# Optimization experiments

Hardware: AMD Instinct MI355X
Metric: run time of the kernel (lower is better)

## Reference

```python
import jax, jax.numpy as jnp
import numpy as np

B, L, D = 2, 2048, 1024
H = 16
DH = D // H  # 64


def rope_tables(seq_len, dim):
    # inv_freq: [dim/2]
    inv_freq = 1.0 / (10000.0 ** (jnp.arange(0, dim, 2, dtype=jnp.float32) / dim))
    t = jnp.arange(seq_len, dtype=jnp.float32)
    freqs = jnp.outer(t, inv_freq)            # [L, dim/2]
    emb = jnp.concatenate([freqs, freqs], -1)  # [L, dim]
    return jnp.cos(emb), jnp.sin(emb)


def rotate_half(x):
    x1, x2 = x[..., : x.shape[-1] // 2], x[..., x.shape[-1] // 2 :]
    return jnp.concatenate([-x2, x1], axis=-1)


def setup_inputs() -> dict:
    key = jax.random.key(0)
    k1, k2, k3 = jax.random.split(key, 3)
    x = jax.random.normal(k1, (B, L, D), dtype=jnp.float32)
    # nn.Linear weight init scale ~ 1/sqrt(fan_in)
    Wqkv = jax.random.normal(k2, (D, 3 * D), dtype=jnp.float32) / np.sqrt(D)
    Wo = jax.random.normal(k3, (D, D), dtype=jnp.float32) / np.sqrt(D)
    return {"x": x, "Wqkv": Wqkv, "Wo": Wo}


def reference(x, Wqkv, Wo):
    b, l, d = x.shape
    qkv = (x @ Wqkv).reshape(b, l, 3, H, DH)
    q, k, v = qkv[:, :, 0], qkv[:, :, 1], qkv[:, :, 2]  # [B, L, H, DH]

    cos, sin = rope_tables(l, DH)          # [L, DH]
    cos = cos[:, None, :]                   # [L, 1, DH] broadcast over heads
    sin = sin[:, None, :]
    q = q * cos + rotate_half(q) * sin
    k = k * cos + rotate_half(k) * sin

    scale = DH ** -0.5
    # full (non-causal) attention, faithful to the source
    scores = jnp.einsum("bqhd,bkhd->bhqk", q, k) * scale   # [B, H, L, L]
    attn = jax.nn.softmax(scores, axis=-1)
    out = jnp.einsum("bhqk,bkhd->bqhd", attn, v)            # [B, L, H, DH]
    out = out.reshape(b, l, d)
    return out @ Wo
```

## Files before the change

### kernel.cpp

```cpp
#include <hip/hip_runtime.h>
#include <hip/hip_bf16.h>

#define B_  2
#define L_  2048
#define D_  1024
#define H_  16
#define DH_ 64
#define M_  (B_*L_)
#define N1_ (3*D_)

#define QSCALE (0.125f * 1.44269504088896340736f)

typedef __bf16 bf16x8 __attribute__((ext_vector_type(8)));
typedef float  f32x4  __attribute__((ext_vector_type(4)));
typedef unsigned short ushort_t;
typedef unsigned short ushort8_t __attribute__((ext_vector_type(8)));
typedef unsigned int   uintx2    __attribute__((ext_vector_type(2)));

#define MFMA16(a,b,c) __builtin_amdgcn_mfma_f32_16x16x32_bf16((a),(b),(c),0,0,0)

__device__ __forceinline__ float4 ld4(const float* p) { return *(const float4*)p; }

__device__ __forceinline__ ushort_t f2bf(float f) {
    union { float f; unsigned int u; } v; v.f = f;
    unsigned int r = (v.u + 0x7FFFu + ((v.u >> 16) & 1u)) >> 16;
    return (ushort_t)r;
}
__device__ __forceinline__ float bf2f(ushort_t u) {
    union { unsigned int u; float f; } v; v.u = ((unsigned int)u) << 16;
    return v.f;
}
__device__ __forceinline__ float exp2_(float x) {
    float r; asm("v_exp_f32 %0, %1" : "=v"(r) : "v"(x)); return r;
}
__device__ __forceinline__ float fract_(float x) {
    float r; asm("v_fract_f32 %0, %1" : "=v"(r) : "v"(x)); return r;
}
__device__ __forceinline__ float sin_rev(float x) {
    float r; asm("v_sin_f32 %0, %1" : "=v"(r) : "v"(x)); return r;
}
__device__ __forceinline__ float cos_rev(float x) {
    float r; asm("v_cos_f32 %0, %1" : "=v"(r) : "v"(x)); return r;
}
__device__ __forceinline__ unsigned cvtpk(float a, float b) {
    unsigned r; asm("v_cvt_pk_bf16_f32 %0, %1, %2" : "=v"(r) : "v"(a), "v"(b)); return r;
}
__device__ __forceinline__ float bperm_f(int byte_addr, float v) {
    union { float f; int i; } u; u.f = v;
    u.i = __builtin_amdgcn_ds_bpermute(byte_addr, u.i);
    return u.f;
}
__device__ __forceinline__ void gload16(const ushort_t* g, ushort_t* l) {
    __builtin_amdgcn_global_load_lds(
        (const __attribute__((address_space(1))) unsigned int*)g,
        (__attribute__((address_space(3))) unsigned int*)l, 16, 0, 0);
}

__global__ __launch_bounds__(256)
void prep(const float* __restrict__ x, const float* __restrict__ Wqkv,
          const float* __restrict__ Wo,
          ushort_t* __restrict__ xb, ushort_t* __restrict__ wqt,
          ushort_t* __restrict__ wot)
{
    __shared__ float vs[64][65];
    const int bid = blockIdx.x, t = threadIdx.x;
    if (bid < 2048) {
        int i = (bid * 256 + t) * 8;
        float4 a = ld4(x + i), b = ld4(x + i + 4);
        ushort8_t o;
        o[0] = f2bf(a.x); o[1] = f2bf(a.y); o[2] = f2bf(a.z); o[3] = f2bf(a.w);
        o[4] = f2bf(b.x); o[5] = f2bf(b.y); o[6] = f2bf(b.z); o[7] = f2bf(b.w);
        *(ushort8_t*)(xb + i) = o;
        return;
    }
    const float* in; ushort_t* out; int nt, kt, N;
    if (bid < 2048 + 768) {
        in = Wqkv; out = wqt; N = N1_;
        nt = (bid - 2048) % 48; kt = (bid - 2048) / 48;
    } else {
        in = Wo; out = wot; N = D_;
        nt = (bid - 2816) % 16; kt = (bid - 2816) / 16;
    }
    #pragma unroll
    for (int i = 0; i < 4; ++i) {
        int idx = t + 256 * i;
        int row = idx >> 4, c4 = idx & 15;
        float4 x4 = ld4(in + (size_t)(kt * 64 + row) * N + nt * 64 + c4 * 4);
        vs[row][c4*4+0] = x4.x; vs[row][c4*4+1] = x4.y;
        vs[row][c4*4+2] = x4.z; vs[row][c4*4+3] = x4.w;
    }
    __syncthreads();
    #pragma unroll
    for (int i = 0; i < 16; ++i) {
        int idx = t + 256 * i;
        int nc = idx >> 6, kc = idx & 63;
        out[(size_t)(nt * 64 + nc) * 1024 + kt * 64 + kc] = f2bf(vs[kc][nc]);
    }
}

template<int EPI, int BM, int NXB, int NWG>
__global__ __launch_bounds__(256)
void bgemm(const ushort_t* __restrict__ A, const ushort_t* __restrict__ Bt,
           float* __restrict__ Cf,
           ushort_t* __restrict__ Qo, ushort_t* __restrict__ Ko, ushort_t* __restrict__ Vo)
{
    constexpr int K  = 1024;
    constexpr int MI = BM / 32;
    __shared__ ushort_t As[BM * 64];
    __shared__ ushort_t Bs[128 * 64];
    const int t  = threadIdx.x;
    const int l  = t & 63, w = t >> 6;
    const int g  = l >> 4, ln = l & 15;
    const int wr = w >> 1, wc = w & 1;
    const int bid = blockIdx.x;
    const int lid = (bid & 7) * (NWG / 8) + (bid >> 3);
    const int m0 = (lid / NXB) * BM, n0 = (lid % NXB) * 128;

    const int srow = w * 8 + (l >> 3);
    const int sch  = (l & 7) ^ (l >> 3);
    const ushort_t* Ag = A  + ((size_t)(m0 + srow)) * K + sch * 8;
    const ushort_t* Bg = Bt + ((size_t)(n0 + srow)) * K + sch * 8;

    f32x4 acc[MI][4];
    #pragma unroll
    for (int mi = 0; mi < MI; ++mi)
        #pragma unroll
        for (int nj = 0; nj < 4; ++nj) acc[mi][nj] = f32x4{0.f, 0.f, 0.f, 0.f};

    for (int kt = 0; kt < K / 64; ++kt) {
        #pragma unroll
        for (int i = 0; i < BM / 32; ++i)
            gload16(Ag + (size_t)i * 32 * K + kt * 64, &As[i * 2048 + w * 512]);
        #pragma unroll
        for (int i = 0; i < 4; ++i)
            gload16(Bg + (size_t)i * 32 * K + kt * 64, &Bs[i * 2048 + w * 512]);
        __syncthreads();

        #pragma unroll
        for (int kk = 0; kk < 2; ++kk) {
            bf16x8 af[MI], bfv[4];
            #pragma unroll
            for (int mi = 0; mi < MI; ++mi) {
                int row  = (BM / 2) * wr + 16 * mi + ln;
                int phys = (4 * kk + g) ^ (ln & 7);
                af[mi] = *(const bf16x8*)&As[row * 64 + phys * 8];
            }
            #pragma unroll
            for (int nj = 0; nj < 4; ++nj) {
                int row  = 64 * wc + 16 * nj + ln;
                int phys = (4 * kk + g) ^ (ln & 7);
                bfv[nj] = *(const bf16x8*)&Bs[row * 64 + phys * 8];
            }
            #pragma unroll
            for (int mi = 0; mi < MI; ++mi)
                #pragma unroll
                for (int nj = 0; nj < 4; ++nj)
                    acc[mi][nj] = MFMA16(af[mi], bfv[nj], acc[mi][nj]);
        }
        __syncthreads();
    }

    if (EPI == 0) {
        #pragma unroll
        for (int mi = 0; mi < MI; ++mi) {
            #pragma unroll
            for (int nj = 0; nj < 4; ++nj) {
                int n = n0 + 64 * wc + 16 * nj + ln;
                #pragma unroll
                for (int r = 0; r < 4; ++r) {
                    int m = m0 + (BM / 2) * wr + 16 * mi + 4 * g + r;
                    Cf[(size_t)m * D_ + n] = acc[mi][nj][r];
                }
            }
        }
    } else {
        const int nb    = n0 + 64 * wc;
        const int which = nb >> 10;
        const int h     = (nb >> 6) & (H_ - 1);
        if (which == 2) {
            #pragma unroll
            for (int mi = 0; mi < MI; ++mi)
                #pragma unroll
                for (int nj = 0; nj < 4; ++nj) {
                    int dh = 16 * nj + ln;
                    #pragma unroll
                    for (int r = 0; r < 4; ++r) {
                        int m = m0 + (BM / 2) * wr + 16 * mi + 4 * g + r;
                        int b = m >> 11, ll = m & (L_ - 1);
                        Vo[((size_t)(b * H_ + h) * DH_ + dh) * L_ + ll] = f2bf(acc[mi][nj][r]);
                    }
                }
        } else {
            ushort_t* base = (which == 0) ? Qo : Ko;
            const float scale = (which == 0) ? QSCALE : 1.0f;
            const float invr0 = exp2_(-(float)ln        * 0.41524101186f) * 0.15915494310f;
            const float invr1 = exp2_(-(float)(16 + ln) * 0.41524101186f) * 0.15915494310f;
            #pragma unroll
            for (int mi = 0; mi < MI; ++mi) {
                #pragma unroll
                for (int r = 0; r < 4; ++r) {
                    int m = m0 + (BM / 2) * wr + 16 * mi + 4 * g + r;
                    int b = m >> 11, ll = m & (L_ - 1);
                    float rv0 = fract_((float)ll * invr0);
                    float rv1 = fract_((float)ll * invr1);
                    float s0 = sin_rev(rv0), c0 = cos_rev(rv0);
                    float s1 = sin_rev(rv1), c1 = cos_rev(rv1);
                    size_t rb = ((size_t)(b * H_ + h) * L_ + ll) * DH_;
                    float a1 = acc[mi][0][r], a2 = acc[mi][2][r];
                    base[rb + ln]      = f2bf((a1 * c0 - a2 * s0) * scale);
                    base[rb + ln + 32] = f2bf((a2 * c0 + a1 * s0) * scale);
                    float b1 = acc[mi][1][r], b2 = acc[mi][3][r];
                    base[rb + 16 + ln]      = f2bf((b1 * c1 - b2 * s1) * scale);
                    base[rb + 16 + ln + 32] = f2bf((b2 * c1 + b1 * s1) * scale);
                }
            }
        }
    }
}

__global__ __launch_bounds__(256)
void attn_mfma(const ushort_t* __restrict__ qb, const ushort_t* __restrict__ kb,
               const ushort_t* __restrict__ vt, ushort_t* __restrict__ ao)
{
    __shared__ ushort_t Ks[128 * 64];
    __shared__ ushort_t Vs[64 * 128];
    __shared__ ushort_t Ps[4][32 * 64];

    const int t    = threadIdx.x;
    const int lane = t & 63, wv = t >> 6;
    const int g    = lane >> 4, ln = lane & 15;
    const int bid  = blockIdx.x;
    const int lid  = (bid & 7) * 64 + (bid >> 3);
    const int bh   = lid >> 4;
    const int q0   = (lid & 15) * 128 + wv * 32;

    const ushort_t* qpA = qb + ((size_t)bh * L_ + q0 + ln) * DH_;
    bf16x8 qf[2][2];
    qf[0][0] = *(const bf16x8*)(qpA + 8 * g);
    qf[0][1] = *(const bf16x8*)(qpA + 32 + 8 * g);
    qf[1][0] = *(const bf16x8*)(qpA + 16 * DH_ + 8 * g);
    qf[1][1] = *(const bf16x8*)(qpA + 16 * DH_ + 32 + 8 * g);

    const ushort_t* kp = kb + (size_t)bh * L_ * DH_;
    const ushort_t* vp = vt + (size_t)bh * DH_ * L_;

    union { ushort8_t u; bf16x8 v; } onesu;
    #pragma unroll
    for (int j = 0; j < 8; ++j) onesu.u[j] = 0x3F80;
    const bf16x8 onesf = onesu.v;

    const int krow8 = lane >> 3;
    const int ksch  = (lane & 7) ^ krow8;
    const int vrow4 = lane >> 4;

    char* Pw = (char*)&Ps[wv][0];
    const int swz = (ln & 7) << 4;

    f32x4 O[2][4], lacc[2];
    #pragma unroll
    for (int h = 0; h < 2; ++h) {
        lacc[h] = f32x4{0.f, 0.f, 0.f, 0.f};
        #pragma unroll
        for (int n = 0; n < 4; ++n) O[h][n] = f32x4{0.f, 0.f, 0.f, 0.f};
    }
    float m_q[2] = {0.f, 0.f};

    auto stage = [&](int tt) {
        #pragma unroll
        for (int i = 0; i < 4; ++i) {
            int row = 32 * wv + 8 * i + krow8;
            gload16(kp + ((size_t)(tt * 128 + row)) * 64 + ksch * 8,
                    &Ks[(32 * wv + 8 * i) * 64]);
        }
        #pragma unroll
        for (int i = 0; i < 4; ++i) {
            int row  = 16 * wv + 4 * i + vrow4;
            int vsch = (lane & 15) ^ ((4 * i + vrow4) & 7);
            gload16(vp + ((size_t)row) * L_ + tt * 128 + vsch * 8,
                    &Vs[(16 * wv + 4 * i) * 128]);
        }
    };

    auto process = [&](int sub) {
        f32x4 S[2][4];
        #pragma unroll
        for (int h = 0; h < 2; ++h)
            #pragma unroll
            for (int n = 0; n < 4; ++n)
                S[h][n] = f32x4{-m_q[h], -m_q[h], -m_q[h], -m_q[h]};
        #pragma unroll
        for (int kk = 0; kk < 2; ++kk) {
            bf16x8 kfv[4];
            #pragma unroll
            for (int n = 0; n < 4; ++n) {
                int row  = 64 * sub + 16 * n + ln;
                int phys = (4 * kk + g) ^ (ln & 7);
                kfv[n] = *(const bf16x8*)&Ks[row * 64 + phys * 8];
            }
            __builtin_amdgcn_s_setprio(1);
            #pragma unroll
            for (int n = 0; n < 4; ++n) S[0][n] = MFMA16(kfv[n], qf[0][kk], S[0][n]);
            #pragma unroll
            for (int n = 0; n < 4; ++n) S[1][n] = MFMA16(kfv[n], qf[1][kk], S[1][n]);
            __builtin_amdgcn_s_setprio(0);
        }

        #pragma unroll
        for (int h = 0; h < 2; ++h) {
            float pmax;
            {
                float a0 = fmaxf(fmaxf(S[h][0][0], S[h][0][1]), fmaxf(S[h][0][2], S[h][0][3]));
                float a1 = fmaxf(fmaxf(S[h][1][0], S[h][1][1]), fmaxf(S[h][1][2], S[h][1][3]));
                float a2 = fmaxf(fmaxf(S[h][2][0], S[h][2][1]), fmaxf(S[h][2][2], S[h][2][3]));
                float a3 = fmaxf(fmaxf(S[h][3][0], S[h][3][1]), fmaxf(S[h][3][2], S[h][3][3]));
                pmax = fmaxf(fmaxf(a0, a1), fmaxf(a2, a3));
            }
            if (!__all(pmax <= 8.0f)) {
                pmax = fmaxf(pmax, __shfl_xor(pmax, 16));
                pmax = fmaxf(pmax, __shfl_xor(pmax, 32));
                m_q[h] += pmax;
                float al = exp2_(-pmax);
                #pragma unroll
                for (int r = 0; r < 4; ++r) {
                    float alr = bperm_f((4 * g + r) * 4, al);
                    lacc[h][r] *= alr;
                    #pragma unroll
                    for (int n = 0; n < 4; ++n) O[h][n][r] *= alr;
                }
                #pragma unroll
                for (int n = 0; n < 4; ++n) S[h][n] = S[h][n] - pmax;
            }

            #pragma unroll
            for (int n = 0; n < 4; ++n) {
                float p0 = exp2_(S[h][n][0]);
                float p1 = exp2_(S[h][n][1]);
                float p2 = exp2_(S[h][n][2]);
                float p3 = exp2_(S[h][n][3]);
                uintx2 wq;
                wq[0] = cvtpk(p0, p1);
                wq[1] = cvtpk(p2, p3);
                *(uintx2*)(Pw + 2048 * h + 128 * ln + ((32 * n + 8 * g) ^ swz)) = wq;
            }
        }

        #pragma unroll
        for (int kk = 0; kk < 2; ++kk) {
            bf16x8 vfv[4];
            #pragma unroll
            for (int n = 0; n < 4; ++n) {
                int row  = 16 * n + ln;
                int phys = 8 * sub + ((4 * kk + g) ^ (ln & 7));
                vfv[n] = *(const bf16x8*)&Vs[row * 128 + phys * 8];
            }
            bf16x8 pa0 = *(const bf16x8*)(Pw + 128 * ln + ((64 * kk + 16 * g) ^ swz));
            bf16x8 pa1 = *(const bf16x8*)(Pw + 2048 + 128 * ln + ((64 * kk + 16 * g) ^ swz));
            __builtin_amdgcn_s_setprio(1);
            #pragma unroll
            for (int n = 0; n < 4; ++n) O[0][n] = MFMA16(pa0, vfv[n], O[0][n]);
            #pragma unroll
            for (int n = 0; n < 4; ++n) O[1][n] = MFMA16(pa1, vfv[n], O[1][n]);
            lacc[0] = MFMA16(pa0, onesf, lacc[0]);
            lacc[1] = MFMA16(pa1, onesf, lacc[1]);
            __builtin_amdgcn_s_setprio(0);
        }
    };

    for (int tt = 0; tt < L_ / 128; ++tt) {
        stage(tt);
        __syncthreads();
        process(0);
        process(1);
        __syncthreads();
    }

    const int b = bh >> 4, hh = bh & 15;
    #pragma unroll
    for (int h = 0; h < 2; ++h) {
        #pragma unroll
        for (int r = 0; r < 4; ++r) {
            float inv = 1.0f / lacc[h][r];
            int ql = q0 + 16 * h + 4 * g + r;
            ushort_t* dst = ao + ((size_t)(b * L_ + ql)) * D_ + hh * 64;
            #pragma unroll
            for (int n = 0; n < 4; ++n)
                dst[16 * n + ln] = f2bf(O[h][n][r] * inv);
        }
    }
}

extern "C" void kernel_launch(void* const* d_in, const int* in_sizes, int n_in,
                              void* d_out, int out_size, void* d_ws, size_t ws_size,
                              hipStream_t stream)
{
    const float* x    = (const float*)d_in[0];
    const float* Wqkv = (const float*)d_in[1];
    const float* Wo   = (const float*)d_in[2];
    float* out = (float*)d_out;

    char* ws = (char*)d_ws;
    ushort_t* xb  = (ushort_t*)(ws);
    ushort_t* wqt = (ushort_t*)(ws + ((size_t) 8 << 20));
    ushort_t* wot = (ushort_t*)(ws + ((size_t)14 << 20));
    ushort_t* qR  = (ushort_t*)(ws + ((size_t)16 << 20));
    ushort_t* kR  = (ushort_t*)(ws + ((size_t)24 << 20));
    ushort_t* vt  = (ushort_t*)(ws + ((size_t)32 << 20));
    ushort_t* ao  = xb;

    prep<<<3072, 256, 0, stream>>>(x, Wqkv, Wo, xb, wqt, wot);
    bgemm<1, 128, N1_/128, 768><<<768, 256, 0, stream>>>(xb, wqt, nullptr, qR, kR, vt);
    attn_mfma<<<512, 256, 0, stream>>>(qR, kR, vt, ao);
    bgemm<0, 64, D_/128, 512><<<512, 256, 0, stream>>>(ao, wot, out, nullptr, nullptr, nullptr);
}
```

Measured before the change: 125.4 us.

## Split attention key range across wave pairs and stage V-transpose epilogue via LDS

The attention kernel now runs 512 threads per block. Each pair of waves shares a 32-query group and splits every 128-key tile into two halves. At the end, the partial max, row-sum and O accumulators are merged through LDS with exp2 rescaling, which doubles the waves available to hide latency. Separately, the QKV GEMM's V epilogue packs results into LDS and writes 16-byte vectorized transposed rows instead of scattered 2-byte stores. The attention change costs a larger LDS footprint, a final merge pass, and extra block barriers.

```diff
diff --git a/kernel.cpp b/kernel.cpp
--- a/kernel.cpp
+++ b/kernel.cpp
@@ -178,18 +178,31 @@
         const int which = nb >> 10;
         const int h     = (nb >> 6) & (H_ - 1);
         if (which == 2) {
-            #pragma unroll
-            for (int mi = 0; mi < MI; ++mi)
-                #pragma unroll
-                for (int nj = 0; nj < 4; ++nj) {
-                    int dh = 16 * nj + ln;
-                    #pragma unroll
-                    for (int r = 0; r < 4; ++r) {
-                        int m = m0 + (BM / 2) * wr + 16 * mi + 4 * g + r;
-                        int b = m >> 11, ll = m & (L_ - 1);
-                        Vo[((size_t)(b * H_ + h) * DH_ + dh) * L_ + ll] = f2bf(acc[mi][nj][r]);
-                    }
+            ushort_t* epi = As + (size_t)w * 1152;
+            const int mb = m0 + (BM / 2) * wr;
+            const int bb = mb >> 11;
+            const int llb = mb & (L_ - 1);
+            #pragma unroll
+            for (int nj = 0; nj < 4; ++nj) {
+                #pragma unroll
+                for (int mi = 0; mi < MI; ++mi) {
+                    uintx2 wq;
+                    wq[0] = cvtpk(acc[mi][nj][0], acc[mi][nj][1]);
+                    wq[1] = cvtpk(acc[mi][nj][2], acc[mi][nj][3]);
+                    int unit = (4 * mi + g) ^ (2 * (ln & 7));
+                    *(uintx2*)&epi[ln * 72 + unit * 4] = wq;
                 }
+                #pragma unroll
+                for (int p = 0; p < 2; ++p) {
+                    int row = (l >> 3) + 8 * p;
+                    int c   = l & 7;
+                    ushort8_t v8 = *(const ushort8_t*)&epi[row * 72 + 8 * c];
+                    int mloc = ((2 * c) ^ (2 * (row & 7))) * 4;
+                    int dh   = 16 * nj + row;
+                    *(ushort8_t*)&Vo[((size_t)(bb * H_ + h) * DH_ + dh) * L_
+                                     + llb + mloc] = v8;
+                }
+            }
         } else {
             ushort_t* base = (which == 0) ? Qo : Ko;
             const float scale = (which == 0) ? QSCALE : 1.0f;
@@ -218,21 +231,22 @@
     }
 }
 
-__global__ __launch_bounds__(256)
+__global__ __launch_bounds__(512, 4)
 void attn_mfma(const ushort_t* __restrict__ qb, const ushort_t* __restrict__ kb,
                const ushort_t* __restrict__ vt, ushort_t* __restrict__ ao)
 {
-    __shared__ ushort_t Ks[128 * 64];
-    __shared__ ushort_t Vs[64 * 128];
-    __shared__ ushort_t Ps[4][32 * 64];
+    __shared__ __attribute__((aligned(16))) char lds[65536];
+    ushort_t* Ks = (ushort_t*)lds;
+    ushort_t* Vs = (ushort_t*)(lds + 16384);
 
     const int t    = threadIdx.x;
     const int lane = t & 63, wv = t >> 6;
     const int g    = lane >> 4, ln = lane & 15;
+    const int qg   = wv >> 1, ks = wv & 1;
     const int bid  = blockIdx.x;
     const int lid  = (bid & 7) * 64 + (bid >> 3);
     const int bh   = lid >> 4;
-    const int q0   = (lid & 15) * 128 + wv * 32;
+    const int q0   = (lid & 15) * 128 + qg * 32;
 
     const ushort_t* qpA = qb + ((size_t)bh * L_ + q0 + ln) * DH_;
     bf16x8 qf[2][2];
@@ -253,7 +267,7 @@
     const int ksch  = (lane & 7) ^ krow8;
     const int vrow4 = lane >> 4;
 
-    char* Pw = (char*)&Ps[wv][0];
+    char* Pw = lds + 32768 + wv * 4096;
     const int swz = (ln & 7) << 4;
 
     f32x4 O[2][4], lacc[2];
@@ -267,17 +281,17 @@
 
     auto stage = [&](int tt) {
         #pragma unroll
-        for (int i = 0; i < 4; ++i) {
-            int row = 32 * wv + 8 * i + krow8;
+        for (int i = 0; i < 2; ++i) {
+            int row = 16 * wv + 8 * i + krow8;
             gload16(kp + ((size_t)(tt * 128 + row)) * 64 + ksch * 8,
-                    &Ks[(32 * wv + 8 * i) * 64]);
-        }
-        #pragma unroll
-        for (int i = 0; i < 4; ++i) {
-            int row  = 16 * wv + 4 * i + vrow4;
+                    &Ks[(16 * wv + 8 * i) * 64]);
+        }
+        #pragma unroll
+        for (int i = 0; i < 2; ++i) {
+            int row  = 8 * wv + 4 * i + vrow4;
             int vsch = (lane & 15) ^ ((4 * i + vrow4) & 7);
             gload16(vp + ((size_t)row) * L_ + tt * 128 + vsch * 8,
-                    &Vs[(16 * wv + 4 * i) * 128]);
+                    &Vs[(8 * wv + 4 * i) * 128]);
         }
     };
 
@@ -369,9 +383,43 @@
     for (int tt = 0; tt < L_ / 128; ++tt) {
         stage(tt);
         __syncthreads();
-        process(0);
-        process(1);
+        process(ks);
         __syncthreads();
+    }
+
+    float* slot = (float*)(lds + qg * 10752) + lane * 42;
+    if (ks == 1) {
+        slot[0] = m_q[0]; slot[1] = m_q[1];
+        #pragma unroll
+        for (int h = 0; h < 2; ++h)
+            #pragma unroll
+            for (int r = 0; r < 4; ++r) slot[2 + 4 * h + r] = lacc[h][r];
+        #pragma unroll
+        for (int h = 0; h < 2; ++h)
+            #pragma unroll
+            for (int n = 0; n < 4; ++n)
+                #pragma unroll
+                for (int r = 0; r < 4; ++r)
+                    slot[10 + 16 * h + 4 * n + r] = O[h][n][r];
+    }
+    __syncthreads();
+    if (ks == 1) return;
+
+    #pragma unroll
+    for (int h = 0; h < 2; ++h) {
+        float m2  = slot[h];
+        float m12 = fmaxf(m_q[h], m2);
+        float a1  = exp2_(m_q[h] - m12);
+        float a2  = exp2_(m2 - m12);
+        #pragma unroll
+        for (int r = 0; r < 4; ++r) {
+            float a1r = bperm_f((4 * g + r) * 4, a1);
+            float a2r = bperm_f((4 * g + r) * 4, a2);
+            lacc[h][r] = lacc[h][r] * a1r + slot[2 + 4 * h + r] * a2r;
+            #pragma unroll
+            for (int n = 0; n < 4; ++n)
+                O[h][n][r] = O[h][n][r] * a1r + slot[10 + 16 * h + 4 * n + r] * a2r;
+        }
     }
 
     const int b = bh >> 4, hh = bh & 15;
@@ -409,6 +457,6 @@
 
     prep<<<3072, 256, 0, stream>>>(x, Wqkv, Wo, xb, wqt, wot);
     bgemm<1, 128, N1_/128, 768><<<768, 256, 0, stream>>>(xb, wqt, nullptr, qR, kR, vt);
-    attn_mfma<<<512, 256, 0, stream>>>(qR, kR, vt, ao);
+    attn_mfma<<<512, 512, 0, stream>>>(qR, kR, vt, ao);
     bgemm<0, 64, D_/128, 512><<<512, 256, 0, stream>>>(ao, wot, out, nullptr, nullptr, nullptr);
 }
```

Measured after the change: 130.5 us. +4.0%, slower.
